# Performance work log

Hardware: AMD Instinct MI355X
Metric: run time of the kernel (lower is better)

## Reference

```python
import math
import jax, jax.numpy as jnp
import numpy as np

B, L, H, D = 1, 2048, 16, 64
M = 24            # nb_features
WINDOW = 128      # local_context / window_size
SCALE = 0.125     # softmax_scale = 1/sqrt(D)
MASK_VAL = -10000.0
EPS = 1e-4        # SBPerformerFeatures eps


def setup_inputs() -> dict:
    key = jax.random.key(0)
    k1, k2 = jax.random.split(key)
    qkv = jax.random.normal(k1, (B, L, 3, H, D), dtype=jnp.float32)
    proj = jax.random.normal(k2, (M, D), dtype=jnp.float32)  # Performer random features
    return {"qkv": qkv, "proj": proj}


def _performer_features(x, proj, is_query):
    # Softmax-kernel random features with separate log scale (scatterbrain SBPerformerFeatures).
    # exp(t*q.k) ~= exp(q_log + k_log) * <q_prime, k_prime>
    dn = math.sqrt(SCALE)
    xs = x * dn                                            # (b,h,l,d)
    x_dash = jnp.einsum('bhld,md->bhlm', xs, proj)         # (b,h,l,m)
    x_norm = 0.5 * jnp.sum(xs * xs, axis=-1, keepdims=True)
    half_log_m = 0.5 * math.log(M)
    if is_query:
        stab = jax.lax.stop_gradient(jnp.max(x_dash, axis=-1, keepdims=True))
        prime = jnp.exp(x_dash - stab) + EPS               # per-row stabilized
        log_scale = stab - x_norm - half_log_m             # (b,h,l,1)
    else:
        stab = jax.lax.stop_gradient(jnp.max(x_dash, axis=(-1, -2), keepdims=True))
        prime = jnp.exp(x_dash - x_norm - stab) + EPS      # norm folded in (needed for cumsum)
        log_scale = stab - half_log_m                      # (b,h,1,1)
    return prime, log_scale


def _band_mask(n):
    idx = jnp.arange(n)
    diff = idx[:, None] - idx[None, :]                     # i - j
    return jnp.where((diff >= 0) & (diff <= WINDOW), 0.0, MASK_VAL)  # (L,L)


def _forward(qkv, proj):
    q, k, v = qkv[:, :, 0], qkv[:, :, 1], qkv[:, :, 2]     # (b,l,h,d)
    q = jnp.transpose(q, (0, 2, 1, 3))                     # (b,h,l,d)
    k = jnp.transpose(k, (0, 2, 1, 3))
    v = jnp.transpose(v, (0, 2, 1, 3))

    # --- GlobalPerformer path ---
    q_prime, q_log = _performer_features(q, proj, True)    # (b,h,l,m), (b,h,l,1)
    k_prime, k_log = _performer_features(k, proj, False)   # (b,h,l,m), (b,h,1,1)
    global_scale = q_log + k_log                           # (b,h,l,1)

    k_cum = jnp.cumsum(k_prime, axis=2)
    global_out_cumsum = jnp.einsum('bhlm,bhlm->bhl', q_prime, k_cum)
    # causal_dot_product: out_i = q'_i . sum_{j<=i} k'_j v_j^T
    kv = jnp.cumsum(k_prime[..., :, None] * v[..., None, :], axis=2)   # (b,h,l,m,d)
    global_out = jnp.einsum('bhlm,bhlmd->bhld', q_prime, kv)

    mask = _band_mask(L)
    p_scores = jnp.einsum('bhme,bhne->bhmn', q_prime, k_prime) * SCALE
    global_qk = jnp.maximum(p_scores + mask[None, None], 0.0)  # masked_fill(<=0, 0)

    # --- Local exact softmax path ---
    scores = jnp.einsum('bhme,bhne->bhmn', q, k) * SCALE
    local_qk = scores + mask[None, None]
    qk_lse = jax.scipy.special.logsumexp(local_qk, axis=-1, keepdims=True)  # (b,h,l,1)

    gqk_sum = jnp.sum(global_qk, axis=-1, keepdims=True)
    global_log_norm = jnp.log(jnp.maximum(global_out_cumsum[..., None] - gqk_sum, 1e-24)) + global_scale
    log_norm = jnp.logaddexp(qk_lse, global_log_norm)      # (b,h,l,1)
    global_prime_scale = jnp.exp(global_scale - log_norm)  # (b,h,l,1)

    local_score = jax.nn.softmax(local_qk - log_norm, axis=-1) - global_qk * global_prime_scale
    out = jnp.einsum('bhmn,bhnd->bhmd', local_score, v) + global_out * global_prime_scale
    return jnp.transpose(out, (0, 2, 1, 3))                # (b,l,h,d)


def reference(qkv, proj):
    return _forward(qkv, proj)
```

## Files before the change

### kernel.cpp

```cpp
#include <hip/hip_runtime.h>
#include <hip/hip_bf16.h>

#define L_SEQ 2048
#define NH 16
#define DH 64
#define NM 24
#define NCH 32
#define SCALE_F 0.125f
#define EPS_F 1e-4f
#define DN_F 0.35355339059327373f
#define HLM_F 1.5890269151739727f

typedef __attribute__((ext_vector_type(8))) short short8v;
typedef __attribute__((ext_vector_type(4))) float f32x4;

__device__ __forceinline__ unsigned short f2bf(float x) {
  unsigned u = __float_as_uint(x);
  u += 0x7FFFu + ((u >> 16) & 1u);
  return (unsigned short)(u >> 16);
}
__device__ __forceinline__ unsigned pk2(float a, float b) {
  return (unsigned)f2bf(a) | ((unsigned)f2bf(b) << 16);
}

__global__ __launch_bounds__(256) void k1_feat(
    const float* __restrict__ qkv, const float* __restrict__ proj,
    float* __restrict__ kdash, float* __restrict__ knorm,
    float* __restrict__ qdash, float* __restrict__ qnorm,
    float* __restrict__ pmax)
{
  __shared__ __attribute__((aligned(16))) float sP[24][68];
  __shared__ __attribute__((aligned(16))) float sX[64][68];
  __shared__ float sRed[256];
  const int c = blockIdx.x, h = blockIdx.y, t = threadIdx.x;
  for (int i = t; i < 24 * 64; i += 256) sP[i >> 6][i & 63] = proj[i];
  float lmax = -1e30f;
  const int r = t >> 2, mg = t & 3;
  for (int qk = 0; qk < 2; ++qk) {
    const int slot = qk ? 0 : 1;
    __syncthreads();
    for (int i = t; i < 4096; i += 256) {
      int rr = i >> 6, d = i & 63;
      int l = c * 64 + rr;
      sX[rr][d] = qkv[(((size_t)l * 3 + slot) * NH + h) * DH + d];
    }
    __syncthreads();
    float acc[6] = {0.f, 0.f, 0.f, 0.f, 0.f, 0.f};
    float sq = 0.f;
    for (int d4 = 0; d4 < 16; ++d4) {
      float4 xv = *(const float4*)&sX[r][d4 * 4];
      sq += xv.x * xv.x; sq += xv.y * xv.y; sq += xv.z * xv.z; sq += xv.w * xv.w;
#pragma unroll
      for (int i = 0; i < 6; ++i) {
        float4 pv = *(const float4*)&sP[mg * 6 + i][d4 * 4];
        acc[i] += xv.x * pv.x; acc[i] += xv.y * pv.y;
        acc[i] += xv.z * pv.z; acc[i] += xv.w * pv.w;
      }
    }
    int l = c * 64 + r;
    float* dsh = qk ? qdash : kdash;
#pragma unroll
    for (int i = 0; i < 6; ++i) {
      float v = acc[i] * DN_F;
      dsh[((size_t)h * L_SEQ + l) * 24 + mg * 6 + i] = v;
      if (!qk) lmax = fmaxf(lmax, v);
    }
    if (mg == 0) (qk ? qnorm : knorm)[h * L_SEQ + l] = 0.5f * SCALE_F * sq;
  }
  sRed[t] = lmax;
  __syncthreads();
#pragma unroll
  for (int s = 128; s > 0; s >>= 1) {
    if (t < s) sRed[t] = fmaxf(sRed[t], sRed[t + s]);
    __syncthreads();
  }
  if (t == 0) pmax[h * 32 + c] = sRed[0];
}

__global__ void k2_stab(const float* __restrict__ pmax, float* __restrict__ stabk)
{
  int h = blockIdx.x, t = threadIdx.x;
  float v = (t < 32) ? pmax[h * 32 + t] : -1e30f;
#pragma unroll
  for (int m = 16; m; m >>= 1) v = fmaxf(v, __shfl_xor(v, m));
  if (t == 0) stabk[h] = v;
}

__global__ __launch_bounds__(256) void k3_kprime(
    const float* __restrict__ qkv, const float* __restrict__ kdash,
    const float* __restrict__ knorm, const float* __restrict__ stabk,
    unsigned* __restrict__ kpw, float* __restrict__ kpfx, float* __restrict__ kvs,
    unsigned* __restrict__ vtw)
{
  __shared__ float sKp[64][25];
  __shared__ __attribute__((aligned(16))) float sV[64][68];
  const int c = blockIdx.x, h = blockIdx.y, t = threadIdx.x;
  const float stab = stabk[h];
  for (int i = t; i < 4096; i += 256) {
    int r = i >> 6, d = i & 63;
    int l = c * 64 + r;
    sV[r][d] = qkv[(((size_t)l * 3 + 2) * NH + h) * DH + d];
  }
  for (int i = t; i < 1536; i += 256) {
    int r = i / 24, m = i % 24;
    int l = c * 64 + r;
    sKp[r][m] = __expf(kdash[((size_t)h * L_SEQ + l) * 24 + m] - knorm[h * L_SEQ + l] - stab) + EPS_F;
  }
  __syncthreads();
  for (int w = t; w < 1024; w += 256) {
    int r = w >> 4, wo = w & 15;
    int l = c * 64 + r;
    float a = (wo < 12) ? sKp[r][2 * wo] : 0.f;
    float bb = (wo < 12) ? sKp[r][2 * wo + 1] : 0.f;
    kpw[((size_t)h * L_SEQ + l) * 16 + wo] = pk2(a, bb);
  }
  for (int w = t; w < 2048; w += 256) {
    int d = w >> 5, lp = w & 31;
    vtw[((size_t)h * NCH + c) * 2048 + d * 32 + lp] = pk2(sV[2 * lp][d], sV[2 * lp + 1][d]);
  }
  if (t < 192) {
    const int m = t % 24, dO = (t / 24) * 8;
    float a0x = 0.f, a0y = 0.f, a0z = 0.f, a0w = 0.f;
    float a1x = 0.f, a1y = 0.f, a1z = 0.f, a1w = 0.f;
    for (int r2 = 0; r2 < 64; ++r2) {
      float kp = sKp[r2][m];
      float4 v0 = *(const float4*)&sV[r2][dO];
      float4 v1 = *(const float4*)&sV[r2][dO + 4];
      a0x += kp * v0.x; a0y += kp * v0.y; a0z += kp * v0.z; a0w += kp * v0.w;
      a1x += kp * v1.x; a1y += kp * v1.y; a1z += kp * v1.z; a1w += kp * v1.w;
    }
    float* dst = kvs + ((size_t)h * NCH + c) * 1536 + m * 64 + dO;
    float4 o0 = {a0x, a0y, a0z, a0w};
    float4 o1 = {a1x, a1y, a1z, a1w};
    *(float4*)dst = o0;
    *(float4*)(dst + 4) = o1;
  }
  if (t < 24) {
    float run = 0.f;
    for (int r2 = 0; r2 < 64; ++r2) {
      run += sKp[r2][t];
      kpfx[((size_t)h * L_SEQ + c * 64 + r2) * 24 + t] = run;
    }
  }
}

__global__ __launch_bounds__(256, 2) void k6_attn(
    const float* __restrict__ qkv, const unsigned* __restrict__ kpw,
    const float* __restrict__ kpfx, const float* __restrict__ kvs,
    const unsigned* __restrict__ vtw,
    const float* __restrict__ qdash, const float* __restrict__ qnorm,
    const float* __restrict__ stabk, float* __restrict__ out)
{
  __shared__ __attribute__((aligned(16))) char lds[62304];
  char* sKW = lds;
  char* sKp = lds + 24576;
  char* sQV = lds + 36864;
  char* sQp = lds + 45056;
  float* sQpF = (float*)(lds + 49152);
  float* sSum = (float*)(lds + 55296);
  float* sGps = sSum + 64;
  float* sRin = sGps + 64;
  float* sKcx = (float*)(lds + 56064);
  float* sPfx = (float*)(lds + 56160);

  const int b = blockIdx.x, h = blockIdx.y, t = threadIdx.x;
  const int wv = t >> 6, lane = t & 63, g = lane >> 4, ln = lane & 15;
  const int keybase = b * 64 - 128;
  const int jmin = (b >= 2) ? 0 : (128 - 64 * b);
  const int rA = wv * 16 + ln;

  for (int w = t; w < 6144; w += 256) {
    int r = w >> 5, dp = w & 31;
    int l = keybase + r; l = l < 0 ? 0 : l;
    const float* s = qkv + (((size_t)l * 3 + 1) * NH + h) * DH + dp * 2;
    *(unsigned*)(sKW + (r * 128 + (((dp * 4)) ^ ((r & 7) << 4)))) = pk2(s[0], s[1]);
  }
  for (int w = t; w < 2048; w += 256) {
    int r = w >> 5, dp = w & 31;
    int l = b * 64 + r;
    const float* s = qkv + (((size_t)l * 3 + 0) * NH + h) * DH + dp * 2;
    *(unsigned*)(sQV + (r * 128 + (((dp * 4)) ^ ((r & 7) << 4)))) = pk2(s[0], s[1]);
  }
  for (int w = t; w < 3072; w += 256) {
    int r = w >> 4, wo = w & 15;
    int l = keybase + r; l = l < 0 ? 0 : l;
    *(unsigned*)(sKp + (r * 64 + (((wo * 4)) ^ ((r & 3) << 4)))) = kpw[((size_t)h * L_SEQ + l) * 16 + wo];
  }
  {
    float accp[6] = {0.f, 0.f, 0.f, 0.f, 0.f, 0.f};
    for (int bp = 0; bp < b; ++bp) {
      const float* src = kvs + ((size_t)h * NCH + bp) * 1536;
#pragma unroll
      for (int j = 0; j < 6; ++j) accp[j] += src[t + j * 256];
    }
#pragma unroll
    for (int j = 0; j < 6; ++j) sPfx[t + j * 256] = accp[j];
  }
  if (t < 24) {
    float runk = 0.f;
    for (int bp = 0; bp < b; ++bp)
      runk += kpfx[((size_t)h * L_SEQ + bp * 64 + 63) * 24 + t];
    sKcx[t] = runk;
  }
  float qlog = 0.f;
  if (t < 64) {
    int r = t, l = b * 64 + r;
    const float* qdp = qdash + ((size_t)h * L_SEQ + l) * 24;
    float qd[24], mx = -1e30f;
#pragma unroll
    for (int m = 0; m < 24; ++m) { qd[m] = qdp[m]; mx = fmaxf(mx, qd[m]); }
    float qpv[24];
#pragma unroll
    for (int m = 0; m < 24; ++m) { qpv[m] = __expf(qd[m] - mx) + EPS_F; sQpF[r * 24 + m] = qpv[m]; }
    qlog = mx - qnorm[h * L_SEQ + l] - HLM_F;
#pragma unroll
    for (int wo = 0; wo < 16; ++wo) {
      float a = (wo < 12) ? qpv[2 * wo] : 0.f;
      float bb = (wo < 12) ? qpv[2 * wo + 1] : 0.f;
      *(unsigned*)(sQp + (r * 64 + (((wo * 4)) ^ ((r & 3) << 4)))) = pk2(a, bb);
    }
  }
  __syncthreads();

  float eF[12][4];
  float rs[4] = {0.f, 0.f, 0.f, 0.f};
  short8v aS0 = *(const short8v*)(sQV + (rA * 128 + ((g * 16) ^ ((rA & 7) << 4))));
  short8v aS1 = *(const short8v*)(sQV + (rA * 128 + ((64 + g * 16) ^ ((rA & 7) << 4))));
#pragma unroll
  for (int nt = 0; nt < 12; ++nt) {
    int rB = nt * 16 + ln;
    short8v b0 = *(const short8v*)(sKW + (rB * 128 + ((g * 16) ^ ((rB & 7) << 4))));
    short8v b1 = *(const short8v*)(sKW + (rB * 128 + ((64 + g * 16) ^ ((rB & 7) << 4))));
    f32x4 acc = {0.f, 0.f, 0.f, 0.f};
    acc = __builtin_amdgcn_mfma_f32_16x16x32_bf16(aS0, b0, acc, 0, 0, 0);
    acc = __builtin_amdgcn_mfma_f32_16x16x32_bf16(aS1, b1, acc, 0, 0, 0);
    int j = nt * 16 + ln;
#pragma unroll
    for (int reg = 0; reg < 4; ++reg) {
      int rl = wv * 16 + g * 4 + reg;
      float e = 0.f;
      if (j >= rl && j <= rl + 128 && j >= jmin) e = __expf(SCALE_F * acc[reg]);
      eF[nt][reg] = e;
      rs[reg] += e;
    }
  }
#pragma unroll
  for (int reg = 0; reg < 4; ++reg) {
    float v = rs[reg];
    v += __shfl_xor(v, 1); v += __shfl_xor(v, 2);
    v += __shfl_xor(v, 4); v += __shfl_xor(v, 8);
    if (ln == 0) sSum[wv * 16 + g * 4 + reg] = v;
  }

  float pF[12][4];
  short8v aP = *(const short8v*)(sQp + (rA * 64 + ((g * 16) ^ ((rA & 3) << 4))));
#pragma unroll
  for (int nt = 0; nt < 12; ++nt) {
    int rB = nt * 16 + ln;
    short8v bp = *(const short8v*)(sKp + (rB * 64 + ((g * 16) ^ ((rB & 3) << 4))));
    f32x4 acc = {0.f, 0.f, 0.f, 0.f};
    acc = __builtin_amdgcn_mfma_f32_16x16x32_bf16(aP, bp, acc, 0, 0, 0);
#pragma unroll
    for (int reg = 0; reg < 4; ++reg) pF[nt][reg] = acc[reg];
  }
  __syncthreads();

  if (t < 64) {
    int r = t, l = b * 64 + r;
    const float* kfc = kpfx + ((size_t)h * L_SEQ + l) * 24;
    int b1i = (b >= 1) ? b - 1 : 0;
    int b2i = (b >= 2) ? b - 2 : 0;
    int rm1 = (r >= 1) ? r - 1 : 0;
    const float* T1p = kpfx + ((size_t)h * L_SEQ + b1i * 64 + 63) * 24;
    const float* T2p = kpfx + ((size_t)h * L_SEQ + b2i * 64 + 63) * 24;
    const float* S2p = kpfx + ((size_t)h * L_SEQ + b2i * 64 + rm1) * 24;
    float f1 = (b >= 1) ? 1.f : 0.f;
    float f2 = (b >= 2) ? 1.f : 0.f;
    float fr = (b >= 2 && r >= 1) ? 1.f : 0.f;
    float psc = 0.f, kcs = 0.f, bnd = 0.f;
#pragma unroll
    for (int m = 0; m < 24; ++m) {
      float qp = sQpF[r * 24 + m];
      float kc = kfc[m];
      psc += qp * kc;
      kcs += qp * sKcx[m];
      bnd += qp * (kc + f1 * T1p[m] + f2 * T2p[m] - fr * S2p[m]);
    }
    float goc = kcs + psc;
    float gqk = SCALE_F * bnd;
    float se = sSum[r];
    float lse = __logf(se);
    float gscale = qlog + stabk[h] - HLM_F;
    float gln = __logf(fmaxf(goc - gqk, 1e-24f)) + gscale;
    float mx2 = fmaxf(lse, gln), mn2 = fminf(lse, gln);
    float lognorm = mx2 + log1pf(__expf(mn2 - mx2));
    sGps[r] = __expf(gscale - lognorm);
    sRin[r] = 1.f / se;
  }
  __syncthreads();

  float gpr[4], rin[4];
#pragma unroll
  for (int reg = 0; reg < 4; ++reg) {
    int rl = wv * 16 + g * 4 + reg;
    gpr[reg] = sGps[rl];
    rin[reg] = sRin[rl];
  }
#pragma unroll
  for (int nt = 0; nt < 12; ++nt) {
    int j = nt * 16 + ln;
#pragma unroll
    for (int reg = 0; reg < 4; ++reg) {
      int rl = wv * 16 + g * 4 + reg;
      bool causal = (j >= 128) && (j <= 128 + rl);
      bool bprev = (j >= rl) && (j < 128) && (j >= jmin);
      float coef = causal ? (1.f - SCALE_F) * gpr[reg] : (bprev ? -SCALE_F * gpr[reg] : 0.f);
      float wgt = eF[nt][reg] * rin[reg] + coef * pF[nt][reg];
      float wn = __shfl_xor(wgt, 1);
      if ((ln & 1) == 0) {
        *(unsigned*)(sKW + (rl * 384 + ((j * 2) ^ ((rl & 7) << 4)))) = pk2(wgt, wn);
      }
    }
  }
  __syncthreads();

  for (int w = t; w < 1024; w += 256) {
    int d = w >> 4, mp = w & 15;
    int m0 = 2 * mp, m1 = m0 + 1;
    float a = (m0 < 24) ? sPfx[m0 * 64 + d] : 0.f;
    float bb = (m1 < 24) ? sPfx[m1 * 64 + d] : 0.f;
    *(unsigned*)(sKp + (d * 64 + ((mp * 4) ^ ((d & 3) << 4)))) = pk2(a, bb);
  }

  f32x4 oF[4];
#pragma unroll
  for (int dt = 0; dt < 4; ++dt) { f32x4 z = {0.f, 0.f, 0.f, 0.f}; oF[dt] = z; }
  for (int vt3 = 0; vt3 < 3; ++vt3) {
    int lt = b - 2 + vt3; lt = lt < 0 ? 0 : lt;
    for (int w = t; w < 2048; w += 256) {
      int d = w >> 5, jp = w & 31;
      *(unsigned*)(sQV + (d * 128 + ((jp * 4) ^ ((d & 7) << 4)))) = vtw[((size_t)h * NCH + lt) * 2048 + d * 32 + jp];
    }
    __syncthreads();
#pragma unroll
    for (int ks = 0; ks < 2; ++ks) {
      short8v aw = *(const short8v*)(sKW + (rA * 384 + ((vt3 * 128 + ks * 64 + g * 16) ^ ((rA & 7) << 4))));
#pragma unroll
      for (int dt = 0; dt < 4; ++dt) {
        int rB = dt * 16 + ln;
        short8v bv = *(const short8v*)(sQV + (rB * 128 + ((ks * 64 + g * 16) ^ ((rB & 7) << 4))));
        oF[dt] = __builtin_amdgcn_mfma_f32_16x16x32_bf16(aw, bv, oF[dt], 0, 0, 0);
      }
    }
    __syncthreads();
  }

  short8v aq = *(const short8v*)(sQp + (rA * 64 + ((g * 16) ^ ((rA & 3) << 4))));
  f32x4 ogF[4];
#pragma unroll
  for (int dt = 0; dt < 4; ++dt) {
    int rB = dt * 16 + ln;
    short8v bg = *(const short8v*)(sKp + (rB * 64 + ((g * 16) ^ ((rB & 3) << 4))));
    f32x4 z = {0.f, 0.f, 0.f, 0.f};
    ogF[dt] = __builtin_amdgcn_mfma_f32_16x16x32_bf16(aq, bg, z, 0, 0, 0);
  }

#pragma unroll
  for (int dt = 0; dt < 4; ++dt) {
    int d = dt * 16 + ln;
#pragma unroll
    for (int reg = 0; reg < 4; ++reg) {
      int rl = wv * 16 + g * 4 + reg;
      int l = b * 64 + rl;
      out[((size_t)l * NH + h) * DH + d] = oF[dt][reg] + gpr[reg] * ogF[dt][reg];
    }
  }
}

extern "C" void kernel_launch(void* const* d_in, const int* in_sizes, int n_in,
                              void* d_out, int out_size, void* d_ws, size_t ws_size,
                              hipStream_t stream)
{
  const float* qkv = (const float*)d_in[0];
  const float* proj = (const float*)d_in[1];
  float* out = (float*)d_out;
  char* ws = (char*)d_ws;

  float* kdash   = (float*)(ws + 0);
  float* qdash   = (float*)(ws + 3145728);
  float* knorm   = (float*)(ws + 6291456);
  float* qnorm   = (float*)(ws + 6422528);
  float* pmax    = (float*)(ws + 6553600);
  float* stabk   = (float*)(ws + 6555648);
  unsigned* kpw  = (unsigned*)(ws + 6556672);
  float* kpfx    = (float*)(ws + 8653824);
  unsigned* vtw  = (unsigned*)(ws + 11799552);
  float* kvs     = (float*)(ws + 15993856);

  k1_feat<<<dim3(32, 16), 256, 0, stream>>>(qkv, proj, kdash, knorm, qdash, qnorm, pmax);
  k2_stab<<<16, 64, 0, stream>>>(pmax, stabk);
  k3_kprime<<<dim3(32, 16), 256, 0, stream>>>(qkv, kdash, knorm, stabk, kpw, kpfx, kvs, vtw);
  k6_attn<<<dim3(32, 16), 256, 0, stream>>>(qkv, kpw, kpfx, kvs, vtw, qdash, qnorm, stabk, out);
}
```

Baseline: 136.7 us.

## Pre-swizzle bf16 Q/K/V in global memory and drop stab kernel

k1 now writes bf16-packed, pre-swizzled copies of K and Q to global memory, and k3 stores kpw and vtw in the same swizzled order. This lets k6 fill shared memory with 16-byte vector copies instead of strided scalar fp32 loads and per-element packing. The separate k2_stab launch is removed: each consumer reduces pmax with wave shuffles, saving one launch. Loads into sX and sV also become float4, at the cost of extra global writes and workspace.

```diff
diff --git a/kernel.cpp b/kernel.cpp
--- a/kernel.cpp
+++ b/kernel.cpp
@@ -22,12 +22,19 @@
 __device__ __forceinline__ unsigned pk2(float a, float b) {
   return (unsigned)f2bf(a) | ((unsigned)f2bf(b) << 16);
 }
+__device__ __forceinline__ float stab_from_pmax(const float* __restrict__ pmax, int h, int t) {
+  float v = pmax[h * 32 + (t & 31)];
+  v = fmaxf(v, __shfl_xor(v, 1));  v = fmaxf(v, __shfl_xor(v, 2));
+  v = fmaxf(v, __shfl_xor(v, 4));  v = fmaxf(v, __shfl_xor(v, 8));
+  v = fmaxf(v, __shfl_xor(v, 16));
+  return v;
+}
 
 __global__ __launch_bounds__(256) void k1_feat(
     const float* __restrict__ qkv, const float* __restrict__ proj,
     float* __restrict__ kdash, float* __restrict__ knorm,
     float* __restrict__ qdash, float* __restrict__ qnorm,
-    float* __restrict__ pmax)
+    float* __restrict__ pmax, unsigned* __restrict__ kbw, unsigned* __restrict__ qbw)
 {
   __shared__ __attribute__((aligned(16))) float sP[24][68];
   __shared__ __attribute__((aligned(16))) float sX[64][68];
@@ -39,12 +46,19 @@
   for (int qk = 0; qk < 2; ++qk) {
     const int slot = qk ? 0 : 1;
     __syncthreads();
-    for (int i = t; i < 4096; i += 256) {
-      int rr = i >> 6, d = i & 63;
+    for (int i = t; i < 1024; i += 256) {
+      int rr = i >> 4, d4 = (i & 15) * 4;
       int l = c * 64 + rr;
-      sX[rr][d] = qkv[(((size_t)l * 3 + slot) * NH + h) * DH + d];
+      *(float4*)&sX[rr][d4] = *(const float4*)(qkv + (((size_t)l * 3 + slot) * NH + h) * DH + d4);
     }
     __syncthreads();
+    unsigned* dstw = qk ? qbw : kbw;
+    for (int w = t; w < 2048; w += 256) {
+      int rr = w >> 5, wo = w & 31;
+      int l = c * 64 + rr;
+      float2 xv = *(const float2*)&sX[rr][2 * wo];
+      dstw[((size_t)h * L_SEQ + l) * 32 + (wo ^ ((rr & 7) << 2))] = pk2(xv.x, xv.y);
+    }
     float acc[6] = {0.f, 0.f, 0.f, 0.f, 0.f, 0.f};
     float sq = 0.f;
     for (int d4 = 0; d4 < 16; ++d4) {
@@ -77,29 +91,20 @@
   if (t == 0) pmax[h * 32 + c] = sRed[0];
 }
 
-__global__ void k2_stab(const float* __restrict__ pmax, float* __restrict__ stabk)
-{
-  int h = blockIdx.x, t = threadIdx.x;
-  float v = (t < 32) ? pmax[h * 32 + t] : -1e30f;
-#pragma unroll
-  for (int m = 16; m; m >>= 1) v = fmaxf(v, __shfl_xor(v, m));
-  if (t == 0) stabk[h] = v;
-}
-
 __global__ __launch_bounds__(256) void k3_kprime(
     const float* __restrict__ qkv, const float* __restrict__ kdash,
-    const float* __restrict__ knorm, const float* __restrict__ stabk,
+    const float* __restrict__ knorm, const float* __restrict__ pmax,
     unsigned* __restrict__ kpw, float* __restrict__ kpfx, float* __restrict__ kvs,
     unsigned* __restrict__ vtw)
 {
   __shared__ float sKp[64][25];
   __shared__ __attribute__((aligned(16))) float sV[64][68];
   const int c = blockIdx.x, h = blockIdx.y, t = threadIdx.x;
-  const float stab = stabk[h];
-  for (int i = t; i < 4096; i += 256) {
-    int r = i >> 6, d = i & 63;
-    int l = c * 64 + r;
-    sV[r][d] = qkv[(((size_t)l * 3 + 2) * NH + h) * DH + d];
+  const float stab = stab_from_pmax(pmax, h, t);
+  for (int i = t; i < 1024; i += 256) {
+    int rr = i >> 4, d4 = (i & 15) * 4;
+    int l = c * 64 + rr;
+    *(float4*)&sV[rr][d4] = *(const float4*)(qkv + (((size_t)l * 3 + 2) * NH + h) * DH + d4);
   }
   for (int i = t; i < 1536; i += 256) {
     int r = i / 24, m = i % 24;
@@ -112,11 +117,11 @@
     int l = c * 64 + r;
     float a = (wo < 12) ? sKp[r][2 * wo] : 0.f;
     float bb = (wo < 12) ? sKp[r][2 * wo + 1] : 0.f;
-    kpw[((size_t)h * L_SEQ + l) * 16 + wo] = pk2(a, bb);
+    kpw[((size_t)h * L_SEQ + l) * 16 + (wo ^ ((r & 3) << 2))] = pk2(a, bb);
   }
   for (int w = t; w < 2048; w += 256) {
-    int d = w >> 5, lp = w & 31;
-    vtw[((size_t)h * NCH + c) * 2048 + d * 32 + lp] = pk2(sV[2 * lp][d], sV[2 * lp + 1][d]);
+    int d = w >> 5, jp = w & 31;
+    vtw[((size_t)h * NCH + c) * 2048 + d * 32 + (jp ^ ((d & 7) << 2))] = pk2(sV[2 * jp][d], sV[2 * jp + 1][d]);
   }
   if (t < 192) {
     const int m = t % 24, dO = (t / 24) * 8;
@@ -145,11 +150,11 @@
 }
 
 __global__ __launch_bounds__(256, 2) void k6_attn(
-    const float* __restrict__ qkv, const unsigned* __restrict__ kpw,
-    const float* __restrict__ kpfx, const float* __restrict__ kvs,
-    const unsigned* __restrict__ vtw,
+    const unsigned* __restrict__ kpw, const float* __restrict__ kpfx,
+    const float* __restrict__ kvs, const unsigned* __restrict__ vtw,
     const float* __restrict__ qdash, const float* __restrict__ qnorm,
-    const float* __restrict__ stabk, float* __restrict__ out)
+    const float* __restrict__ pmax, const unsigned* __restrict__ kbw,
+    const unsigned* __restrict__ qbw, float* __restrict__ out)
 {
   __shared__ __attribute__((aligned(16))) char lds[62304];
   char* sKW = lds;
@@ -169,23 +174,22 @@
   const int jmin = (b >= 2) ? 0 : (128 - 64 * b);
   const int rA = wv * 16 + ln;
 
-  for (int w = t; w < 6144; w += 256) {
-    int r = w >> 5, dp = w & 31;
+  for (int w = t; w < 1536; w += 256) {
+    int r = w >> 3, q4 = w & 7;
     int l = keybase + r; l = l < 0 ? 0 : l;
-    const float* s = qkv + (((size_t)l * 3 + 1) * NH + h) * DH + dp * 2;
-    *(unsigned*)(sKW + (r * 128 + (((dp * 4)) ^ ((r & 7) << 4)))) = pk2(s[0], s[1]);
-  }
-  for (int w = t; w < 2048; w += 256) {
-    int r = w >> 5, dp = w & 31;
+    *(uint4*)(sKW + r * 128 + q4 * 16) = *(const uint4*)(kbw + ((size_t)h * L_SEQ + l) * 32 + q4 * 4);
+  }
+  for (int w = t; w < 512; w += 256) {
+    int r = w >> 3, q4 = w & 7;
     int l = b * 64 + r;
-    const float* s = qkv + (((size_t)l * 3 + 0) * NH + h) * DH + dp * 2;
-    *(unsigned*)(sQV + (r * 128 + (((dp * 4)) ^ ((r & 7) << 4)))) = pk2(s[0], s[1]);
-  }
-  for (int w = t; w < 3072; w += 256) {
-    int r = w >> 4, wo = w & 15;
+    *(uint4*)(sQV + r * 128 + q4 * 16) = *(const uint4*)(qbw + ((size_t)h * L_SEQ + l) * 32 + q4 * 4);
+  }
+  for (int w = t; w < 768; w += 256) {
+    int r = w >> 2, q4 = w & 3;
     int l = keybase + r; l = l < 0 ? 0 : l;
-    *(unsigned*)(sKp + (r * 64 + (((wo * 4)) ^ ((r & 3) << 4)))) = kpw[((size_t)h * L_SEQ + l) * 16 + wo];
-  }
+    *(uint4*)(sKp + r * 64 + q4 * 16) = *(const uint4*)(kpw + ((size_t)h * L_SEQ + l) * 16 + q4 * 4);
+  }
+  const float stab = stab_from_pmax(pmax, h, t);
   {
     float accp[6] = {0.f, 0.f, 0.f, 0.f, 0.f, 0.f};
     for (int bp = 0; bp < b; ++bp) {
@@ -290,7 +294,7 @@
     float gqk = SCALE_F * bnd;
     float se = sSum[r];
     float lse = __logf(se);
-    float gscale = qlog + stabk[h] - HLM_F;
+    float gscale = qlog + stab - HLM_F;
     float gln = __logf(fmaxf(goc - gqk, 1e-24f)) + gscale;
     float mx2 = fmaxf(lse, gln), mn2 = fminf(lse, gln);
     float lognorm = mx2 + log1pf(__expf(mn2 - mx2));
@@ -337,9 +341,8 @@
   for (int dt = 0; dt < 4; ++dt) { f32x4 z = {0.f, 0.f, 0.f, 0.f}; oF[dt] = z; }
   for (int vt3 = 0; vt3 < 3; ++vt3) {
     int lt = b - 2 + vt3; lt = lt < 0 ? 0 : lt;
-    for (int w = t; w < 2048; w += 256) {
-      int d = w >> 5, jp = w & 31;
-      *(unsigned*)(sQV + (d * 128 + ((jp * 4) ^ ((d & 7) << 4)))) = vtw[((size_t)h * NCH + lt) * 2048 + d * 32 + jp];
+    for (int w = t; w < 512; w += 256) {
+      *(uint4*)(sQV + w * 16) = *(const uint4*)(vtw + ((size_t)h * NCH + lt) * 2048 + w * 4);
     }
     __syncthreads();
 #pragma unroll
@@ -391,14 +394,14 @@
   float* knorm   = (float*)(ws + 6291456);
   float* qnorm   = (float*)(ws + 6422528);
   float* pmax    = (float*)(ws + 6553600);
-  float* stabk   = (float*)(ws + 6555648);
-  unsigned* kpw  = (unsigned*)(ws + 6556672);
-  float* kpfx    = (float*)(ws + 8653824);
-  unsigned* vtw  = (unsigned*)(ws + 11799552);
-  float* kvs     = (float*)(ws + 15993856);
-
-  k1_feat<<<dim3(32, 16), 256, 0, stream>>>(qkv, proj, kdash, knorm, qdash, qnorm, pmax);
-  k2_stab<<<16, 64, 0, stream>>>(pmax, stabk);
-  k3_kprime<<<dim3(32, 16), 256, 0, stream>>>(qkv, kdash, knorm, stabk, kpw, kpfx, kvs, vtw);
-  k6_attn<<<dim3(32, 16), 256, 0, stream>>>(qkv, kpw, kpfx, kvs, vtw, qdash, qnorm, stabk, out);
-}
+  unsigned* kbw  = (unsigned*)(ws + 6555648);
+  unsigned* qbw  = (unsigned*)(ws + 10749952);
+  unsigned* kpw  = (unsigned*)(ws + 14944256);
+  float* kpfx    = (float*)(ws + 17041408);
+  unsigned* vtw  = (unsigned*)(ws + 20187136);
+  float* kvs     = (float*)(ws + 24381440);
+
+  k1_feat<<<dim3(32, 16), 256, 0, stream>>>(qkv, proj, kdash, knorm, qdash, qnorm, pmax, kbw, qbw);
+  k3_kprime<<<dim3(32, 16), 256, 0, stream>>>(qkv, kdash, knorm, pmax, kpw, kpfx, kvs, vtw);
+  k6_attn<<<dim3(32, 16), 256, 0, stream>>>(kpw, kpfx, kvs, vtw, qdash, qnorm, pmax, kbw, qbw, out);
+}
```

Result: faster. 125.7 us (-8.0%).
